# Optimization experiments

Measured on AMD Instinct MI355X. Metric: run time of the kernel, lower is better.

The kernel has to match this reference:

```python
import jax, jax.numpy as jnp
import numpy as np

NUM_GROUPS = 16   # static upper bound on group ids (actual ids in [0, 12))
MIN_COUNT = 10    # min_subgroup_count


def setup_inputs() -> dict:
    key = jax.random.key(0)
    ks = jax.random.split(key, 7)
    B = 32768
    N = 16777216  # dataset_size
    probs = jax.random.uniform(ks[0], (B,), dtype=jnp.float32)
    labels = jax.random.randint(ks[1], (B,), 0, 2, dtype=jnp.int32)
    groups = jax.random.randint(ks[2], (B,), 0, 12, dtype=jnp.int32)
    indices = jax.random.randint(ks[3], (B,), 0, N, dtype=jnp.int32)
    # persistent buffers, pre-filled with valid mid-epoch state
    score_buffer = jax.random.uniform(ks[4], (N,), dtype=jnp.float32)
    label_buffer = jax.random.randint(ks[5], (N,), 0, 2, dtype=jnp.int32)
    group_buffer = jax.random.randint(ks[6], (N,), 0, 12, dtype=jnp.int32)
    return {"probs": probs, "labels": labels, "groups": groups, "indices": indices,
            "score_buffer": score_buffer, "label_buffer": label_buffer,
            "group_buffer": group_buffer}


def reference(probs, labels, groups, indices, score_buffer, label_buffer, group_buffer):
    # scatter current batch into dataset-sized buffers (functional clone + write)
    scores = score_buffer.at[indices].set(probs)
    labs = label_buffer.at[indices].set(labels)
    grps = group_buffer.at[indices].set(groups)

    valid = (~jnp.isnan(scores)) & (labs >= 0) & (grps >= 0)
    scores = jnp.where(valid, scores, 0.0)        # kill NaNs before weighted sums
    seg = jnp.where(valid, grps, 0)               # invalid rows get weight 0 anyway

    def group_var(lab_val):
        # per-group mean of scores restricted to (valid & label==lab_val),
        # then unbiased variance across groups meeting the min-count threshold
        w = (valid & (labs == lab_val)).astype(scores.dtype)
        sums = jax.ops.segment_sum(scores * w, seg, num_segments=NUM_GROUPS)
        cnts = jax.ops.segment_sum(w, seg, num_segments=NUM_GROUPS)
        avg = sums / jnp.maximum(cnts, 1.0)
        incl = (cnts >= MIN_COUNT).astype(scores.dtype)
        n = incl.sum()
        mean = (avg * incl).sum() / jnp.maximum(n, 1.0)
        var = (incl * (avg - mean) ** 2).sum() / jnp.maximum(n - 1.0, 1.0)  # ddof=1
        return var, n

    pos_var, n_pos = group_var(1)
    neg_var, n_neg = group_var(0)
    pos_ok = n_pos >= 2.0
    neg_ok = n_neg >= 2.0
    loss = jnp.where(pos_ok & neg_ok, 0.5 * (pos_var + neg_var),
                     jnp.where(pos_ok, pos_var,
                               jnp.where(neg_ok, neg_var, 0.0)))
    return loss
```

## Files before the change

### kernel.cpp

```cpp
#include <hip/hip_runtime.h>
#include <hip/hip_bf16.h>


#define TBL   65536u
#define TBLM  (TBL - 1u)
#define NGR   12
#define NBK   24
#define NCOL  25
#define NTHR  256
#define CHUNK 16384
#define ITER  (CHUNK / 4 / NTHR)
#define DEPTH1 4
#define DEPTH2 8
#define MINC  10.0

__device__ __forceinline__ unsigned hash_idx(unsigned idx) {
    return (idx * 2654435761u) & TBLM;
}

__global__ void k_vote(const int* __restrict__ indices,
                       unsigned long long* __restrict__ table,
                       unsigned* __restrict__ bitmap, int B) {
    int b = blockIdx.x * blockDim.x + threadIdx.x;
    if (b >= B) return;
    unsigned idx = (unsigned)indices[b];
    atomicOr(&bitmap[idx >> 5], 1u << (idx & 31u));
    unsigned long long key = ((unsigned long long)(idx + 1u)) << 32;
    unsigned long long val = key | (unsigned long long)(unsigned)b;
    unsigned slot = hash_idx(idx);
    for (;;) {
        unsigned long long prev = atomicCAS(&table[slot], 0ULL, val);
        if (prev == 0ULL) return;
        if ((prev >> 32) == (unsigned long long)(idx + 1u)) {
            atomicMax(&table[slot], val);
            return;
        }
        slot = (slot + 1u) & TBLM;
    }
}

__global__ void k_resolve(const unsigned long long* __restrict__ table,
                          const float* __restrict__ probs,
                          const int* __restrict__ labels,
                          const int* __restrict__ groups,
                          float4* __restrict__ tbl2) {
    int s = blockIdx.x * blockDim.x + threadIdx.x;
    unsigned long long e = table[s];
    unsigned hi = (unsigned)(e >> 32);
    float4 r = make_float4(0.f, 0.f, 0.f, 0.f);
    if (hi) {
        int b = (int)(e & 0xffffffffu);
        r.x = probs[b];
        r.y = __int_as_float(labels[b]);
        r.z = __int_as_float(groups[b]);
        r.w = __uint_as_float(hi);
    }
    tbl2[s] = r;
}

__device__ __forceinline__ void apply_ovr(int idx, float& s, int& l, int& g,
        const float4* __restrict__ tbl2) {
    unsigned slot = hash_idx((unsigned)idx);
    unsigned hi = (unsigned)idx + 1u;
    for (;;) {
        float4 r = tbl2[slot];
        if (__float_as_uint(r.w) == hi) {
            s = r.x; l = __float_as_int(r.y); g = __float_as_int(r.z);
            return;
        }
        slot = (slot + 1u) & TBLM;
    }
}

__device__ __forceinline__ float ovr_s(int idx,
        const float4* __restrict__ tbl2) {
    unsigned slot = hash_idx((unsigned)idx);
    unsigned hi = (unsigned)idx + 1u;
    for (;;) {
        float4 r = tbl2[slot];
        if (__float_as_uint(r.w) == hi) return r.x;
        slot = (slot + 1u) & TBLM;
    }
}

__device__ __forceinline__ void quad_p1(float* __restrict__ row,
        unsigned* __restrict__ bstr32,
        float4 s4, int4 l4, int4 g4, unsigned bits, int v,
        const float4* __restrict__ tbl2) {
    float ss[4] = {s4.x, s4.y, s4.z, s4.w};
    int   ll[4] = {l4.x, l4.y, l4.z, l4.w};
    int   gg[4] = {g4.x, g4.y, g4.z, g4.w};
    if (bits & 0xFu) {
#pragma unroll
        for (int e = 0; e < 4; ++e)
            if ((bits >> e) & 1u)
                apply_ovr((v << 2) + e, ss[e], ll[e], gg[e], tbl2);
    }
    float val[4]; int bkt[4];
#pragma unroll
    for (int e = 0; e < 4; ++e) {
        bool valid = (ss[e] == ss[e]) && ((unsigned)ll[e] < 2u) &&
                     ((unsigned)gg[e] < (unsigned)NGR);
        bkt[e] = valid ? (gg[e] * 2 + ll[e]) : NBK;
        val[e] = valid ? ss[e] : 0.f;
    }
    bstr32[v] = (unsigned)bkt[0] | ((unsigned)bkt[1] << 8) |
                ((unsigned)bkt[2] << 16) | ((unsigned)bkt[3] << 24);
#define MRG(i, j) { bool m_ = (bkt[i] == bkt[j]); \
                    val[i] += m_ ? val[j] : 0.f;  \
                    bkt[j] = m_ ? NBK : bkt[j];   \
                    val[j] = m_ ? 0.f : val[j]; }
    MRG(0,1) MRG(0,2) MRG(0,3) MRG(1,2) MRG(1,3) MRG(2,3)
#undef MRG
    float a0 = row[bkt[0]], a1 = row[bkt[1]], a2 = row[bkt[2]], a3 = row[bkt[3]];
    row[bkt[0]] = a0 + val[0];
    row[bkt[1]] = a1 + val[1];
    row[bkt[2]] = a2 + val[2];
    row[bkt[3]] = a3 + val[3];
}

__global__ __launch_bounds__(NTHR) void k_pass1(
        const float* __restrict__ sb, const int* __restrict__ lb,
        const int* __restrict__ gb, const unsigned* __restrict__ bitmap,
        const float4* __restrict__ tbl2,
        float* __restrict__ bsum, unsigned char* __restrict__ bstream,
        int n, int nblk) {
    __shared__ float s_acc[NTHR * NCOL];
    int tid = threadIdx.x, blk = blockIdx.x;
    for (int i = tid; i < NTHR * NCOL; i += NTHR) s_acc[i] = 0.f;
    __syncthreads();
    float* row = &s_acc[tid * NCOL];
    unsigned* bstr32 = (unsigned*)bstream;
    int vbase = (blk * CHUNK) >> 2, nv = n >> 2;
    if (vbase + (CHUNK >> 2) <= nv) {
        int v0 = vbase + tid;
        float4 ps[DEPTH1]; int4 pl[DEPTH1], pg[DEPTH1]; unsigned pb[DEPTH1];
#pragma unroll
        for (int d = 0; d < DEPTH1; ++d) {
            int v = v0 + d * NTHR;
            ps[d] = ((const float4*)sb)[v];
            pl[d] = ((const int4*)lb)[v];
            pg[d] = ((const int4*)gb)[v];
            pb[d] = bitmap[v >> 3];
        }
        unsigned sh = (unsigned)((v0 & 7) * 4);
#pragma unroll
        for (int it = 0; it < ITER; ++it) {
            int d = it & (DEPTH1 - 1);
            int v = v0 + it * NTHR;
            float4 s4 = ps[d]; int4 l4 = pl[d], g4 = pg[d];
            unsigned bits = pb[d] >> sh;
            if (it + DEPTH1 < ITER) {
                int w = v + DEPTH1 * NTHR;
                ps[d] = ((const float4*)sb)[w];
                pl[d] = ((const int4*)lb)[w];
                pg[d] = ((const int4*)gb)[w];
                pb[d] = bitmap[w >> 3];
            }
            asm volatile("" ::: "memory");
            quad_p1(row, bstr32, s4, l4, g4, bits, v, tbl2);
        }
    } else {
        for (int it = 0; it < ITER; ++it) {
            int v = vbase + it * NTHR + tid;
            if (v >= nv) break;
            float4 s4 = ((const float4*)sb)[v];
            int4   l4 = ((const int4*)lb)[v];
            int4   g4 = ((const int4*)gb)[v];
            unsigned bits = bitmap[v >> 3] >> ((v & 7) * 4);
            quad_p1(row, bstr32, s4, l4, g4, bits, v, tbl2);
        }
    }
    if (blk == nblk - 1) {
        for (int i = (nv << 2) + tid; i < n; i += NTHR) {
            float s = sb[i]; int l = lb[i], g = gb[i];
            if ((bitmap[i >> 5] >> (i & 31)) & 1u)
                apply_ovr(i, s, l, g, tbl2);
            bool valid = (s == s) && ((unsigned)l < 2u) && ((unsigned)g < (unsigned)NGR);
            int bk = valid ? (g * 2 + l) : NBK;
            bstream[i] = (unsigned char)bk;
            row[bk] += valid ? s : 0.f;
        }
    }
    __syncthreads();
    if (tid < NBK * 8) {
        int bkt = tid >> 3, sub = tid & 7;
        float sm = 0.f;
        for (int j = 0; j < 32; ++j) sm += s_acc[(sub * 32 + j) * NCOL + bkt];
        for (int d = 4; d >= 1; d >>= 1) sm += __shfl_down(sm, d, 8);
        if (!sub) bsum[bkt * nblk + blk] = sm;
    }
}

__global__ void k_scan(const float* __restrict__ bsum,
                       float* __restrict__ bpref, int nblk) {
    __shared__ double sc[NTHR];
    int t = threadIdx.x, k = blockIdx.x;
    const float* src = bsum  + (size_t)k * nblk;
    float*       dst = bpref + (size_t)k * nblk;
    double carry = 0.0;
    for (int s0 = 0; s0 < nblk; s0 += 4 * NTHR) {
        int i0 = s0 + 4 * t;
        float x0 = (i0 + 0 < nblk) ? src[i0 + 0] : 0.f;
        float x1 = (i0 + 1 < nblk) ? src[i0 + 1] : 0.f;
        float x2 = (i0 + 2 < nblk) ? src[i0 + 2] : 0.f;
        float x3 = (i0 + 3 < nblk) ? src[i0 + 3] : 0.f;
        double p0 = (double)x0, p1 = p0 + x1, p2 = p1 + x2, tot = p2 + x3;
        sc[t] = tot;
        __syncthreads();
        for (int st = 1; st < NTHR; st <<= 1) {
            double a = (t >= st) ? sc[t - st] : 0.0;
            __syncthreads();
            sc[t] += a;
            __syncthreads();
        }
        double excl = carry + sc[t] - tot;
        if (i0 + 0 < nblk) dst[i0 + 0] = (float)excl;
        if (i0 + 1 < nblk) dst[i0 + 1] = (float)(excl + p0);
        if (i0 + 2 < nblk) dst[i0 + 2] = (float)(excl + p1);
        if (i0 + 3 < nblk) dst[i0 + 3] = (float)(excl + p2);
        double bt = sc[NTHR - 1];
        __syncthreads();
        carry += bt;
    }
}

__device__ __forceinline__ double aload_d(const double* p) {
    unsigned long long u = __hip_atomic_load((const unsigned long long*)p,
                              __ATOMIC_RELAXED, __HIP_MEMORY_SCOPE_AGENT);
    return __longlong_as_double((long long)u);
}

__device__ __forceinline__ void quad_p2(float2* __restrict__ row,
        const float2* __restrict__ s_model,
        float4 s4, unsigned b4, unsigned obits, int v, int base,
        const float4* __restrict__ tbl2) {
    float ss[4] = {s4.x, s4.y, s4.z, s4.w};
    if (obits & 0xFu) {
#pragma unroll
        for (int e = 0; e < 4; ++e)
            if ((obits >> e) & 1u) ss[e] = ovr_s((v << 2) + e, tbl2);
    }
    float cv[4], cn[4]; int bkt[4];
#pragma unroll
    for (int e = 0; e < 4; ++e) {
        int idx = (v << 2) + e;
        int bk = (int)((b4 >> (8 * e)) & 0xFFu);
        float s = ss[e];
        float2 m = s_model[bk];
        float S = fmaf(m.y, (float)(idx - base), m.x);
        float T = S + s;
        unsigned ue = __float_as_uint(T) & 0x7f800000u;
        float c;
        if (ue < (24u << 23)) c = s;
        else {
            unsigned ub = ue - (23u << 23);
            float u    = __uint_as_float(ub);
            float uinv = __uint_as_float((254u << 23) - ub);
            c = u * rintf(s * uinv);
        }
        bool valid = bk < NBK;
        bkt[e] = bk;
        cv[e] = valid ? c : 0.f;
        cn[e] = valid ? 1.f : 0.f;
    }
#define MRG(i, j) { bool m_ = (bkt[i] == bkt[j]); \
                    cv[i] += m_ ? cv[j] : 0.f;    \
                    cn[i] += m_ ? cn[j] : 0.f;    \
                    bkt[j] = m_ ? NBK : bkt[j];   \
                    cv[j] = m_ ? 0.f : cv[j];     \
                    cn[j] = m_ ? 0.f : cn[j]; }
    MRG(0,1) MRG(0,2) MRG(0,3) MRG(1,2) MRG(1,3) MRG(2,3)
#undef MRG
    float2 a0 = row[bkt[0]], a1 = row[bkt[1]], a2 = row[bkt[2]], a3 = row[bkt[3]];
    a0.x += cv[0]; a0.y += cn[0];
    a1.x += cv[1]; a1.y += cn[1];
    a2.x += cv[2]; a2.y += cn[2];
    a3.x += cv[3]; a3.y += cn[3];
    row[bkt[0]] = a0; row[bkt[1]] = a1; row[bkt[2]] = a2; row[bkt[3]] = a3;
}

__global__ __launch_bounds__(NTHR) void k_pass2(
        const float* __restrict__ sb,
        const unsigned char* __restrict__ bstream,
        const unsigned* __restrict__ bitmap,
        const float4* __restrict__ tbl2,
        const float* __restrict__ bsum, const float* __restrict__ bpref,
        double* __restrict__ acc_sum, double* __restrict__ acc_cnt,
        unsigned* __restrict__ done, float* __restrict__ out,
        int n, int nblk) {
    __shared__ float2 s_acc[NTHR * NCOL];
    __shared__ float2 s_model[NCOL];
    int tid = threadIdx.x, blk = blockIdx.x;
    for (int i = tid; i < NTHR * NCOL; i += NTHR) s_acc[i] = make_float2(0.f, 0.f);
    if (tid < NBK)
        s_model[tid] = make_float2(bpref[tid * nblk + blk],
                                   bsum[tid * nblk + blk] * (1.0f / CHUNK));
    if (tid == NBK) s_model[NBK] = make_float2(0.f, 0.f);
    __syncthreads();
    float2* row = &s_acc[tid * NCOL];
    const unsigned* bstr32 = (const unsigned*)bstream;
    int base = blk * CHUNK;
    int vbase = base >> 2, nv = n >> 2;
    if (vbase + (CHUNK >> 2) <= nv) {
        int v0 = vbase + tid;
        float4 ps[DEPTH2]; unsigned pk[DEPTH2], pb[DEPTH2];
#pragma unroll
        for (int d = 0; d < DEPTH2; ++d) {
            int v = v0 + d * NTHR;
            ps[d] = ((const float4*)sb)[v];
            pk[d] = bstr32[v];
            pb[d] = bitmap[v >> 3];
        }
        unsigned sh = (unsigned)((v0 & 7) * 4);
#pragma unroll
        for (int it = 0; it < ITER; ++it) {
            int d = it & (DEPTH2 - 1);
            int v = v0 + it * NTHR;
            float4 s4 = ps[d]; unsigned b4 = pk[d];
            unsigned bits = pb[d] >> sh;
            if (it + DEPTH2 < ITER) {
                int w = v + DEPTH2 * NTHR;
                ps[d] = ((const float4*)sb)[w];
                pk[d] = bstr32[w];
                pb[d] = bitmap[w >> 3];
            }
            asm volatile("" ::: "memory");
            quad_p2(row, s_model, s4, b4, bits, v, base, tbl2);
        }
    } else {
        for (int it = 0; it < ITER; ++it) {
            int v = vbase + it * NTHR + tid;
            if (v >= nv) break;
            float4 s4 = ((const float4*)sb)[v];
            unsigned b4 = bstr32[v];
            unsigned bits = bitmap[v >> 3] >> ((v & 7) * 4);
            quad_p2(row, s_model, s4, b4, bits, v, base, tbl2);
        }
    }
    if (blk == nblk - 1) {
        for (int i = (nv << 2) + tid; i < n; i += NTHR) {
            float s = sb[i];
            int bk = (int)bstream[i];
            if ((bitmap[i >> 5] >> (i & 31)) & 1u)
                s = ovr_s(i, tbl2);
            float2 m = s_model[bk];
            float S = fmaf(m.y, (float)(i - base), m.x);
            float T = S + s;
            unsigned ue = __float_as_uint(T) & 0x7f800000u;
            float c;
            if (ue < (24u << 23)) c = s;
            else {
                unsigned ub = ue - (23u << 23);
                float u    = __uint_as_float(ub);
                float uinv = __uint_as_float((254u << 23) - ub);
                c = u * rintf(s * uinv);
            }
            bool valid = bk < NBK;
            float2 a = row[bk];
            a.x += valid ? c : 0.f;
            a.y += valid ? 1.f : 0.f;
            row[bk] = a;
        }
    }
    __syncthreads();
    if (tid < NBK * 8) {
        int bkt = tid >> 3, sub = tid & 7;
        float sm = 0.f, cc = 0.f;
        for (int j = 0; j < 32; ++j) {
            float2 a = s_acc[(sub * 32 + j) * NCOL + bkt];
            sm += a.x; cc += a.y;
        }
        for (int d = 4; d >= 1; d >>= 1) {
            sm += __shfl_down(sm, d, 8);
            cc += __shfl_down(cc, d, 8);
        }
        if (!sub) {
            atomicAdd(&acc_sum[bkt], (double)sm);
            atomicAdd(&acc_cnt[bkt], (double)cc);
        }
    }
    __syncthreads();
    if (tid == 0) {
        __threadfence();
        unsigned r = __hip_atomic_fetch_add(done, 1u, __ATOMIC_ACQ_REL,
                                            __HIP_MEMORY_SCOPE_AGENT);
        if (r == (unsigned)(gridDim.x - 1)) {
            double var[2], nn[2];
            for (int l = 0; l < 2; ++l) {
                double avg[NGR];
                double ncnt = 0.0, s = 0.0;
                for (int g = 0; g < NGR; ++g) {
                    double c  = aload_d(&acc_cnt[g * 2 + l]);
                    double sm = aload_d(&acc_sum[g * 2 + l]);
                    double a = sm / fmax(c, 1.0);
                    avg[g] = a;
                    if (c >= MINC) { ncnt += 1.0; s += a; }
                }
                double mean = s / fmax(ncnt, 1.0), v = 0.0;
                for (int g = 0; g < NGR; ++g) {
                    double c = aload_d(&acc_cnt[g * 2 + l]);
                    if (c >= MINC) { double d = avg[g] - mean; v += d * d; }
                }
                var[l] = v / fmax(ncnt - 1.0, 1.0);
                nn[l] = ncnt;
            }
            bool p = nn[1] >= 2.0, q = nn[0] >= 2.0;
            double loss = (p && q) ? 0.5 * (var[1] + var[0])
                        : (p ? var[1] : (q ? var[0] : 0.0));
            out[0] = (float)loss;
        }
    }
}

extern "C" void kernel_launch(void* const* d_in, const int* in_sizes, int n_in,
                              void* d_out, int out_size, void* d_ws, size_t ws_size,
                              hipStream_t stream) {
    const float* probs   = (const float*)d_in[0];
    const int*   labels  = (const int*)d_in[1];
    const int*   groups  = (const int*)d_in[2];
    const int*   indices = (const int*)d_in[3];
    const float* sb      = (const float*)d_in[4];
    const int*   lb      = (const int*)d_in[5];
    const int*   gb      = (const int*)d_in[6];
    int B = in_sizes[0];
    int n = in_sizes[4];
    int nblk   = (n + CHUNK - 1) / CHUNK;
    int nwords = (n + 31) / 32;

    char* ws = (char*)d_ws;
    size_t off = 0;
    unsigned long long* table = (unsigned long long*)(ws + off); off += (size_t)TBL * 8;
    unsigned* bitmap  = (unsigned*)(ws + off); off += (size_t)nwords * 4;
    off = (off + 15) & ~(size_t)15;
    double*   acc_sum = (double*)(ws + off);   off += NBK * 8;
    double*   acc_cnt = (double*)(ws + off);   off += NBK * 8;
    unsigned* done    = (unsigned*)(ws + off); off += 16;
    size_t zero_bytes = off;
    float4*   tbl2    = (float4*)(ws + off);   off += (size_t)TBL * 16;
    unsigned char* bstream = (unsigned char*)(ws + off);
    off += ((size_t)n + 15) & ~(size_t)15;
    float*    bsum    = (float*)(ws + off);    off += (size_t)nblk * NBK * 4;
    float*    bpref   = (float*)(ws + off);    off += (size_t)nblk * NBK * 4;

    hipMemsetAsync(d_ws, 0, zero_bytes, stream);

    dim3 bblk((B + NTHR - 1) / NTHR);
    hipLaunchKernelGGL(k_vote, bblk, dim3(NTHR), 0, stream,
                       indices, table, bitmap, B);
    hipLaunchKernelGGL(k_resolve, dim3(TBL / NTHR), dim3(NTHR), 0, stream,
                       table, probs, labels, groups, tbl2);
    hipLaunchKernelGGL(k_pass1, dim3(nblk), dim3(NTHR), 0, stream,
                       sb, lb, gb, bitmap, tbl2, bsum, bstream, n, nblk);
    hipLaunchKernelGGL(k_scan, dim3(NBK), dim3(NTHR), 0, stream,
                       bsum, bpref, nblk);
    hipLaunchKernelGGL(k_pass2, dim3(nblk), dim3(NTHR), 0, stream,
                       sb, bstream, bitmap, tbl2, bsum, bpref,
                       acc_sum, acc_cnt, done, (float*)d_out, n, nblk);
}
```

Before: 325.7 us.

## Shrink pass-2 LDS with ushort counters, batch loads, raise occupancy

Pass-2 per-thread count histograms move from float (interleaved in a float2) to a separate unsigned short array, so the shared-memory footprint drops from about 51KB to about 39KB per block. The rolling-register prefetch pipelines in both passes are replaced by batched groups of four loads followed by processing. Both kernels also get a launch_bounds minimum of four blocks per SM. Together these aim to raise occupancy and cut register pressure, so more waves can hide memory latency. The cost is less explicit prefetch depth and 16-bit LDS read-modify-write traffic, and the extra waves only help if LDS allows them: pass 1 still uses about 25KB per block, and pass 2 may still fit only a few blocks per CU.

```diff
diff --git a/kernel.cpp b/kernel.cpp
--- a/kernel.cpp
+++ b/kernel.cpp
@@ -7,11 +7,11 @@
 #define NGR   12
 #define NBK   24
 #define NCOL  25
+#define CCOL  26
 #define NTHR  256
 #define CHUNK 16384
 #define ITER  (CHUNK / 4 / NTHR)
-#define DEPTH1 4
-#define DEPTH2 8
+#define UNR   4
 #define MINC  10.0
 
 __device__ __forceinline__ unsigned hash_idx(unsigned idx) {
@@ -119,7 +119,7 @@
     row[bkt[3]] = a3 + val[3];
 }
 
-__global__ __launch_bounds__(NTHR) void k_pass1(
+__global__ __launch_bounds__(NTHR, 4) void k_pass1(
         const float* __restrict__ sb, const int* __restrict__ lb,
         const int* __restrict__ gb, const unsigned* __restrict__ bitmap,
         const float4* __restrict__ tbl2,
@@ -134,31 +134,24 @@
     int vbase = (blk * CHUNK) >> 2, nv = n >> 2;
     if (vbase + (CHUNK >> 2) <= nv) {
         int v0 = vbase + tid;
-        float4 ps[DEPTH1]; int4 pl[DEPTH1], pg[DEPTH1]; unsigned pb[DEPTH1];
-#pragma unroll
-        for (int d = 0; d < DEPTH1; ++d) {
-            int v = v0 + d * NTHR;
-            ps[d] = ((const float4*)sb)[v];
-            pl[d] = ((const int4*)lb)[v];
-            pg[d] = ((const int4*)gb)[v];
-            pb[d] = bitmap[v >> 3];
-        }
         unsigned sh = (unsigned)((v0 & 7) * 4);
 #pragma unroll
-        for (int it = 0; it < ITER; ++it) {
-            int d = it & (DEPTH1 - 1);
-            int v = v0 + it * NTHR;
-            float4 s4 = ps[d]; int4 l4 = pl[d], g4 = pg[d];
-            unsigned bits = pb[d] >> sh;
-            if (it + DEPTH1 < ITER) {
-                int w = v + DEPTH1 * NTHR;
-                ps[d] = ((const float4*)sb)[w];
-                pl[d] = ((const int4*)lb)[w];
-                pg[d] = ((const int4*)gb)[w];
-                pb[d] = bitmap[w >> 3];
+        for (int m = 0; m < ITER / UNR; ++m) {
+            float4 s4[UNR]; int4 l4[UNR], g4[UNR]; unsigned bm[UNR];
+#pragma unroll
+            for (int u = 0; u < UNR; ++u) {
+                int v = v0 + (m * UNR + u) * NTHR;
+                s4[u] = ((const float4*)sb)[v];
+                l4[u] = ((const int4*)lb)[v];
+                g4[u] = ((const int4*)gb)[v];
+                bm[u] = bitmap[v >> 3];
             }
             asm volatile("" ::: "memory");
-            quad_p1(row, bstr32, s4, l4, g4, bits, v, tbl2);
+#pragma unroll
+            for (int u = 0; u < UNR; ++u) {
+                int v = v0 + (m * UNR + u) * NTHR;
+                quad_p1(row, bstr32, s4[u], l4[u], g4[u], bm[u] >> sh, v, tbl2);
+            }
         }
     } else {
         for (int it = 0; it < ITER; ++it) {
@@ -231,7 +224,8 @@
     return __longlong_as_double((long long)u);
 }
 
-__device__ __forceinline__ void quad_p2(float2* __restrict__ row,
+__device__ __forceinline__ void quad_p2(float* __restrict__ row,
+        unsigned short* __restrict__ crow,
         const float2* __restrict__ s_model,
         float4 s4, unsigned b4, unsigned obits, int v, int base,
         const float4* __restrict__ tbl2) {
@@ -241,7 +235,7 @@
         for (int e = 0; e < 4; ++e)
             if ((obits >> e) & 1u) ss[e] = ovr_s((v << 2) + e, tbl2);
     }
-    float cv[4], cn[4]; int bkt[4];
+    float cv[4]; int bkt[4], cn[4];
 #pragma unroll
     for (int e = 0; e < 4; ++e) {
         int idx = (v << 2) + e;
@@ -262,25 +256,30 @@
         bool valid = bk < NBK;
         bkt[e] = bk;
         cv[e] = valid ? c : 0.f;
-        cn[e] = valid ? 1.f : 0.f;
+        cn[e] = valid ? 1 : 0;
     }
 #define MRG(i, j) { bool m_ = (bkt[i] == bkt[j]); \
                     cv[i] += m_ ? cv[j] : 0.f;    \
-                    cn[i] += m_ ? cn[j] : 0.f;    \
+                    cn[i] += m_ ? cn[j] : 0;      \
                     bkt[j] = m_ ? NBK : bkt[j];   \
                     cv[j] = m_ ? 0.f : cv[j];     \
-                    cn[j] = m_ ? 0.f : cn[j]; }
+                    cn[j] = m_ ? 0 : cn[j]; }
     MRG(0,1) MRG(0,2) MRG(0,3) MRG(1,2) MRG(1,3) MRG(2,3)
 #undef MRG
-    float2 a0 = row[bkt[0]], a1 = row[bkt[1]], a2 = row[bkt[2]], a3 = row[bkt[3]];
-    a0.x += cv[0]; a0.y += cn[0];
-    a1.x += cv[1]; a1.y += cn[1];
-    a2.x += cv[2]; a2.y += cn[2];
-    a3.x += cv[3]; a3.y += cn[3];
-    row[bkt[0]] = a0; row[bkt[1]] = a1; row[bkt[2]] = a2; row[bkt[3]] = a3;
-}
-
-__global__ __launch_bounds__(NTHR) void k_pass2(
+    float a0 = row[bkt[0]], a1 = row[bkt[1]], a2 = row[bkt[2]], a3 = row[bkt[3]];
+    row[bkt[0]] = a0 + cv[0];
+    row[bkt[1]] = a1 + cv[1];
+    row[bkt[2]] = a2 + cv[2];
+    row[bkt[3]] = a3 + cv[3];
+    unsigned short c0 = crow[bkt[0]], c1 = crow[bkt[1]],
+                   c2 = crow[bkt[2]], c3 = crow[bkt[3]];
+    crow[bkt[0]] = (unsigned short)(c0 + cn[0]);
+    crow[bkt[1]] = (unsigned short)(c1 + cn[1]);
+    crow[bkt[2]] = (unsigned short)(c2 + cn[2]);
+    crow[bkt[3]] = (unsigned short)(c3 + cn[3]);
+}
+
+__global__ __launch_bounds__(NTHR, 4) void k_pass2(
         const float* __restrict__ sb,
         const unsigned char* __restrict__ bstream,
         const unsigned* __restrict__ bitmap,
@@ -289,44 +288,42 @@
         double* __restrict__ acc_sum, double* __restrict__ acc_cnt,
         unsigned* __restrict__ done, float* __restrict__ out,
         int n, int nblk) {
-    __shared__ float2 s_acc[NTHR * NCOL];
+    __shared__ float s_accv[NTHR * NCOL];
+    __shared__ unsigned short s_cnt[NTHR * CCOL];
     __shared__ float2 s_model[NCOL];
     int tid = threadIdx.x, blk = blockIdx.x;
-    for (int i = tid; i < NTHR * NCOL; i += NTHR) s_acc[i] = make_float2(0.f, 0.f);
+    for (int i = tid; i < NTHR * NCOL; i += NTHR) s_accv[i] = 0.f;
+    for (int i = tid; i < NTHR * CCOL; i += NTHR) s_cnt[i] = 0;
     if (tid < NBK)
         s_model[tid] = make_float2(bpref[tid * nblk + blk],
                                    bsum[tid * nblk + blk] * (1.0f / CHUNK));
     if (tid == NBK) s_model[NBK] = make_float2(0.f, 0.f);
     __syncthreads();
-    float2* row = &s_acc[tid * NCOL];
+    float* row = &s_accv[tid * NCOL];
+    unsigned short* crow = &s_cnt[tid * CCOL];
     const unsigned* bstr32 = (const unsigned*)bstream;
     int base = blk * CHUNK;
     int vbase = base >> 2, nv = n >> 2;
     if (vbase + (CHUNK >> 2) <= nv) {
         int v0 = vbase + tid;
-        float4 ps[DEPTH2]; unsigned pk[DEPTH2], pb[DEPTH2];
-#pragma unroll
-        for (int d = 0; d < DEPTH2; ++d) {
-            int v = v0 + d * NTHR;
-            ps[d] = ((const float4*)sb)[v];
-            pk[d] = bstr32[v];
-            pb[d] = bitmap[v >> 3];
-        }
         unsigned sh = (unsigned)((v0 & 7) * 4);
 #pragma unroll
-        for (int it = 0; it < ITER; ++it) {
-            int d = it & (DEPTH2 - 1);
-            int v = v0 + it * NTHR;
-            float4 s4 = ps[d]; unsigned b4 = pk[d];
-            unsigned bits = pb[d] >> sh;
-            if (it + DEPTH2 < ITER) {
-                int w = v + DEPTH2 * NTHR;
-                ps[d] = ((const float4*)sb)[w];
-                pk[d] = bstr32[w];
-                pb[d] = bitmap[w >> 3];
+        for (int m = 0; m < ITER / UNR; ++m) {
+            float4 s4[UNR]; unsigned pk[UNR], bm[UNR];
+#pragma unroll
+            for (int u = 0; u < UNR; ++u) {
+                int v = v0 + (m * UNR + u) * NTHR;
+                s4[u] = ((const float4*)sb)[v];
+                pk[u] = bstr32[v];
+                bm[u] = bitmap[v >> 3];
             }
             asm volatile("" ::: "memory");
-            quad_p2(row, s_model, s4, b4, bits, v, base, tbl2);
+#pragma unroll
+            for (int u = 0; u < UNR; ++u) {
+                int v = v0 + (m * UNR + u) * NTHR;
+                quad_p2(row, crow, s_model, s4[u], pk[u], bm[u] >> sh,
+                        v, base, tbl2);
+            }
         }
     } else {
         for (int it = 0; it < ITER; ++it) {
@@ -335,7 +332,7 @@
             float4 s4 = ((const float4*)sb)[v];
             unsigned b4 = bstr32[v];
             unsigned bits = bitmap[v >> 3] >> ((v & 7) * 4);
-            quad_p2(row, s_model, s4, b4, bits, v, base, tbl2);
+            quad_p2(row, crow, s_model, s4, b4, bits, v, base, tbl2);
         }
     }
     if (blk == nblk - 1) {
@@ -357,19 +354,18 @@
                 c = u * rintf(s * uinv);
             }
             bool valid = bk < NBK;
-            float2 a = row[bk];
-            a.x += valid ? c : 0.f;
-            a.y += valid ? 1.f : 0.f;
-            row[bk] = a;
+            row[bk] += valid ? c : 0.f;
+            crow[bk] = (unsigned short)(crow[bk] + (valid ? 1 : 0));
         }
     }
     __syncthreads();
     if (tid < NBK * 8) {
         int bkt = tid >> 3, sub = tid & 7;
-        float sm = 0.f, cc = 0.f;
+        float sm = 0.f; unsigned cc = 0;
         for (int j = 0; j < 32; ++j) {
-            float2 a = s_acc[(sub * 32 + j) * NCOL + bkt];
-            sm += a.x; cc += a.y;
+            int t2 = sub * 32 + j;
+            sm += s_accv[t2 * NCOL + bkt];
+            cc += s_cnt[t2 * CCOL + bkt];
         }
         for (int d = 4; d >= 1; d >>= 1) {
             sm += __shfl_down(sm, d, 8);
```

Result: faster. 305.1 us (-6.3%).
